# Performance work log

Hardware: AMD Instinct MI355X
Metric: run time of the kernel (lower is better)

Reference implementation:

```python
import jax, jax.numpy as jnp
import numpy as np

D_MODEL, N_HEADS, D_FF = 1024, 16, 4096
D_HEAD = D_MODEL // N_HEADS
B, S = 2, 2048
EPS = 1e-5


def setup_inputs() -> dict:
    key = jax.random.key(0)
    ks = jax.random.split(key, 12)
    sd = 1.0 / np.sqrt(D_MODEL)
    return {
        "x": jax.random.normal(ks[0], (B, S, D_MODEL), jnp.float32),
        "relative_bias": jax.random.normal(ks[1], (1, N_HEADS, S, S), jnp.float32),
        # attention projections, stored as (in, out) so y = x @ W
        "wq": jax.random.normal(ks[2], (D_MODEL, D_MODEL), jnp.float32) * sd,
        "wk": jax.random.normal(ks[3], (D_MODEL, D_MODEL), jnp.float32) * sd,
        "wv": jax.random.normal(ks[4], (D_MODEL, D_MODEL), jnp.float32) * sd,
        "wo": jax.random.normal(ks[5], (D_MODEL, D_MODEL), jnp.float32) * sd,
        "wo_b": jnp.zeros((D_MODEL,), jnp.float32),
        # FFN
        "w1": jax.random.normal(ks[6], (D_MODEL, D_FF), jnp.float32) * sd,
        "b1": jnp.zeros((D_FF,), jnp.float32),
        "w2": jax.random.normal(ks[7], (D_FF, D_MODEL), jnp.float32) * (1.0 / np.sqrt(D_FF)),
        "b2": jnp.zeros((D_MODEL,), jnp.float32),
        # LayerNorms
        "ln1_g": jnp.ones((D_MODEL,), jnp.float32),
        "ln1_b": jnp.zeros((D_MODEL,), jnp.float32),
        "ln2_g": jnp.ones((D_MODEL,), jnp.float32),
        "ln2_b": jnp.zeros((D_MODEL,), jnp.float32),
    }


def _layernorm(x, g, b):
    mu = jnp.mean(x, axis=-1, keepdims=True)
    var = jnp.mean(jnp.square(x - mu), axis=-1, keepdims=True)
    return (x - mu) * jax.lax.rsqrt(var + EPS) * g + b


def _attn(x, relative_bias, wq, wk, wv, wo, wo_b):
    b, s, d = x.shape
    # (B,S,D) -> (B,H,S,Dh)
    def split_heads(t):
        return t.reshape(b, s, N_HEADS, D_HEAD).transpose(0, 2, 1, 3)
    q = split_heads(x @ wq)
    k = split_heads(x @ wk)
    v = split_heads(x @ wv)
    scores = jnp.einsum("bhqd,bhkd->bhqk", q, k) / np.sqrt(D_HEAD) + relative_bias
    attn = jax.nn.softmax(scores, axis=-1)
    ctx = jnp.einsum("bhqk,bhkd->bhqd", attn, v)
    ctx = ctx.transpose(0, 2, 1, 3).reshape(b, s, d)
    return ctx @ wo + wo_b


def _ffn(x, w1, b1, w2, b2):
    return jax.nn.gelu(x @ w1 + b1, approximate=False) @ w2 + b2


def reference(x, relative_bias, wq, wk, wv, wo, wo_b, w1, b1, w2, b2,
              ln1_g, ln1_b, ln2_g, ln2_b):
    x = x + _attn(_layernorm(x, ln1_g, ln1_b), relative_bias, wq, wk, wv, wo, wo_b)
    x = x + _ffn(_layernorm(x, ln2_g, ln2_b), w1, b1, w2, b2)
    return x
```

## Files before the change

kernel.cpp:

```cpp
#include <hip/hip_runtime.h>
#include <hip/hip_bf16.h>
#include <stdint.h>

typedef unsigned short u16;
typedef __bf16 bf16x8 __attribute__((ext_vector_type(8)));
typedef u16   u16x8  __attribute__((ext_vector_type(8)));
typedef u16   u16x4  __attribute__((ext_vector_type(4)));
typedef u16   u16x2  __attribute__((ext_vector_type(2)));
typedef float f32x4  __attribute__((ext_vector_type(4)));

__device__ __forceinline__ u16 f2bf(float f) {
  union { float f; uint32_t u; } v; v.f = f;
  uint32_t r = v.u + 0x7fffu + ((v.u >> 16) & 1u);
  return (u16)(r >> 16);
}

typedef __attribute__((address_space(1))) void gvoid_t;
typedef __attribute__((address_space(3))) void lvoid_t;
__device__ __forceinline__ void gload_lds16(const void* g, void* l) {
  __builtin_amdgcn_global_load_lds((gvoid_t*)g, (lvoid_t*)l, 16, 0, 0);
}

template<int CTRL>
__device__ __forceinline__ float dpp_f(float x) {
  int i = __builtin_bit_cast(int, x);
  i = __builtin_amdgcn_update_dpp(i, i, CTRL, 0xF, 0xF, true);
  return __builtin_bit_cast(float, i);
}
__device__ __forceinline__ float rowmax16(float x) {
  x = fmaxf(x, dpp_f<0x128>(x));
  x = fmaxf(x, dpp_f<0x124>(x));
  x = fmaxf(x, dpp_f<0x122>(x));
  x = fmaxf(x, dpp_f<0x121>(x));
  return x;
}
__device__ __forceinline__ float rowsum16(float x) {
  x += dpp_f<0x128>(x);
  x += dpp_f<0x124>(x);
  x += dpp_f<0x122>(x);
  x += dpp_f<0x121>(x);
  return x;
}

__global__ __launch_bounds__(256)
void ln_kernel(const float* __restrict__ x, const float* __restrict__ g,
               const float* __restrict__ b, u16* __restrict__ out) {
  const int row = blockIdx.x;
  const int tid = threadIdx.x;
  const float* xr = x + (size_t)row * 1024;
  f32x4 v = *(const f32x4*)&xr[tid * 4];
  float s = v[0] + v[1] + v[2] + v[3];
  float q = v[0]*v[0] + v[1]*v[1] + v[2]*v[2] + v[3]*v[3];
  #pragma unroll
  for (int o = 32; o > 0; o >>= 1) { s += __shfl_xor(s, o); q += __shfl_xor(q, o); }
  __shared__ float ss[4], qq[4];
  if ((tid & 63) == 0) { ss[tid >> 6] = s; qq[tid >> 6] = q; }
  __syncthreads();
  s = ss[0] + ss[1] + ss[2] + ss[3];
  q = qq[0] + qq[1] + qq[2] + qq[3];
  float mu = s * (1.0f / 1024.0f);
  float var = q * (1.0f / 1024.0f) - mu * mu;
  float rstd = rsqrtf(var + 1e-5f);
  u16x4 o4;
  #pragma unroll
  for (int i = 0; i < 4; ++i)
    o4[i] = f2bf((v[i] - mu) * rstd * g[tid * 4 + i] + b[tid * 4 + i]);
  *(u16x4*)&out[(size_t)row * 1024 + tid * 4] = o4;
}

__global__ __launch_bounds__(256)
void transpose_cast(const float* __restrict__ W, u16* __restrict__ Wt, int K, int N) {
  __shared__ float t[32][33];
  const int n0 = blockIdx.x * 32, k0 = blockIdx.y * 32;
  const int tx = threadIdx.x & 31, ty = threadIdx.x >> 5;
  #pragma unroll
  for (int i = 0; i < 4; ++i)
    t[ty + 8*i][tx] = W[(size_t)(k0 + ty + 8*i) * N + n0 + tx];
  __syncthreads();
  #pragma unroll
  for (int i = 0; i < 4; ++i)
    Wt[(size_t)(n0 + ty + 8*i) * K + k0 + tx] = f2bf(t[tx][ty + 8*i]);
}

template<int EPI>
__global__ __launch_bounds__(256, 2)
void gemm_bt(const u16* __restrict__ A, const u16* __restrict__ Bt,
             void* __restrict__ out, const float* __restrict__ bias,
             const float* __restrict__ resid, int M, int N, int K) {
  __shared__ u16 As[128 * 32];
  __shared__ u16 Bs[128 * 32];
  const int tid = threadIdx.x;
  const int w = tid >> 6, l = tid & 63;
  const int bm = blockIdx.x * 128, bn = blockIdx.y * 128;
  const int wr = (w >> 1) * 64, wc = (w & 1) * 64;
  const int l15 = l & 15, lhi = l >> 4;
  f32x4 acc[4][4] = {};

  const int r4 = tid >> 2;
  const int c8 = (tid & 3) * 8;
  const u16* ga0 = A  + (size_t)(bm + r4) * K + c8;
  const u16* ga1 = ga0 + (size_t)64 * K;
  const u16* gb0 = Bt + (size_t)(bn + r4) * K + c8;
  const u16* gb1 = gb0 + (size_t)64 * K;
  u16* lA0 = &As[(w * 16) * 32];
  u16* lA1 = &As[(64 + w * 16) * 32];
  u16* lB0 = &Bs[(w * 16) * 32];
  u16* lB1 = &Bs[(64 + w * 16) * 32];

  const int arow = (wr + l15) * 32 + lhi * 8;
  const int brow = (wc + l15) * 32 + lhi * 8;

  for (int k0 = 0; k0 < K; k0 += 32) {
    gload_lds16(ga0 + k0, lA0);
    gload_lds16(ga1 + k0, lA1);
    gload_lds16(gb0 + k0, lB0);
    gload_lds16(gb1 + k0, lB1);
    __syncthreads();
    bf16x8 a[4], b[4];
    #pragma unroll
    for (int m = 0; m < 4; ++m) a[m] = *(const bf16x8*)&As[arow + m * 16 * 32];
    #pragma unroll
    for (int n = 0; n < 4; ++n) b[n] = *(const bf16x8*)&Bs[brow + n * 16 * 32];
    #pragma unroll
    for (int m = 0; m < 4; ++m)
      #pragma unroll
      for (int n = 0; n < 4; ++n)
        acc[m][n] = __builtin_amdgcn_mfma_f32_16x16x32_bf16(a[m], b[n], acc[m][n], 0, 0, 0);
    __syncthreads();
  }

  #pragma unroll
  for (int m = 0; m < 4; ++m) {
    #pragma unroll
    for (int n = 0; n < 4; ++n) {
      #pragma unroll
      for (int r = 0; r < 4; ++r) {
        const int grow = bm + wr + m * 16 + lhi * 4 + r;
        const int gcol = bn + wc + n * 16 + l15;
        float vv = acc[m][n][r];
        if constexpr (EPI >= 1) vv += bias[gcol];
        if constexpr (EPI == 1) vv = 0.5f * vv * (1.0f + erff(vv * 0.70710678118f));
        if constexpr (EPI == 2) {
          vv += resid[(size_t)grow * N + gcol];
          ((float*)out)[(size_t)grow * N + gcol] = vv;
        } else {
          ((u16*)out)[(size_t)grow * N + gcol] = f2bf(vv);
        }
      }
    }
  }
}

#define SWZ(row) ((((row) & 7) ^ (((row) >> 3) & 7)) << 3)

__global__ __launch_bounds__(256)
void attn_kernel(const u16* __restrict__ qkv, const float* __restrict__ bias,
                 u16* __restrict__ ctx) {
  const int qt = blockIdx.x;
  const int bh = blockIdx.y;
  const int b = bh >> 4, h = bh & 15;
  const int tid = threadIdx.x, w = tid >> 6, l = tid & 63;
  const int l15 = l & 15, lhi = l >> 4;
  const size_t ld = 3072;
  const float L2E = 1.44269504f;

  __shared__ u16 Kl[4096];
  __shared__ u16 Vt[4096];
  __shared__ u16 Pl[4][1024];

  const u16* qp = qkv;
  const u16* kp = qkv + 1024;
  const u16* vp = qkv + 2048;

  const int key2 = (tid >> 3) * 2, dg8 = (tid & 7) * 8;
  const u16* kbase = kp + ((size_t)b * 2048 + key2) * ld + h * 64 + dg8;
  const u16* vbase = vp + ((size_t)b * 2048 + key2) * ld + h * 64 + dg8;

  bf16x8 qf0, qf1;
  {
    const u16* qrow = qp + ((size_t)b * 2048 + qt * 64 + w * 16 + l15) * ld + h * 64 + lhi * 8;
    qf0 = *(const bf16x8*)qrow;
    qf1 = *(const bf16x8*)(qrow + 32);
  }

  const float* bg0 = bias + ((size_t)h * 2048 + qt * 64 + w * 16 + lhi * 4) * 2048 + l15;

  float m_run[4], s_run[4];
  f32x4 octx[4] = {};
  #pragma unroll
  for (int r = 0; r < 4; ++r) { m_run[r] = -1e30f; s_run[r] = 0.f; }

  u16x8 kpf[2], vpf[2];
  float bf[16];

  auto load_kv = [&](int kv) {
    kpf[0] = *(const u16x8*)(kbase + (size_t)kv * ld);
    kpf[1] = *(const u16x8*)(kbase + (size_t)(kv + 1) * ld);
    vpf[0] = *(const u16x8*)(vbase + (size_t)kv * ld);
    vpf[1] = *(const u16x8*)(vbase + (size_t)(kv + 1) * ld);
  };
  auto load_bias = [&](int kv) {
    #pragma unroll
    for (int r = 0; r < 4; ++r)
      #pragma unroll
      for (int nf = 0; nf < 4; ++nf)
        bf[r * 4 + nf] = bg0[(size_t)r * 2048 + kv + nf * 16];
  };
  auto store_kv = [&]() {
    *(u16x8*)&Kl[(key2)     * 64 + (dg8 ^ SWZ(key2))]     = kpf[0];
    *(u16x8*)&Kl[(key2 + 1) * 64 + (dg8 ^ SWZ(key2 + 1))] = kpf[1];
    #pragma unroll
    for (int i = 0; i < 8; ++i) {
      const int d = dg8 + i;
      u16x2 vq = { vpf[0][i], vpf[1][i] };
      *(u16x2*)&Vt[d * 64 + (key2 ^ SWZ(d))] = vq;
    }
  };

  load_kv(0);
  load_bias(0);
  store_kv();
  __syncthreads();

  for (int it = 0; it < 32; ++it) {
    const int kv0 = it * 64;
    const bool pf = it < 31;
    if (pf) load_kv(kv0 + 64);

    f32x4 sa[4] = {};
    #pragma unroll
    for (int nf = 0; nf < 4; ++nf) {
      const int row = nf * 16 + l15;
      const int s = SWZ(row);
      bf16x8 kf0 = *(const bf16x8*)&Kl[row * 64 + ((lhi * 8) ^ s)];
      bf16x8 kf1 = *(const bf16x8*)&Kl[row * 64 + ((32 + lhi * 8) ^ s)];
      sa[nf] = __builtin_amdgcn_mfma_f32_16x16x32_bf16(qf0, kf0, sa[nf], 0, 0, 0);
      sa[nf] = __builtin_amdgcn_mfma_f32_16x16x32_bf16(qf1, kf1, sa[nf], 0, 0, 0);
    }

    float p[4][4];
    #pragma unroll
    for (int r = 0; r < 4; ++r)
      #pragma unroll
      for (int nf = 0; nf < 4; ++nf)
        p[r][nf] = fmaf(sa[nf][r], 0.125f, bf[r * 4 + nf]);
    if (pf) load_bias(kv0 + 64);

    #pragma unroll
    for (int r = 0; r < 4; ++r) {
      float mx = fmaxf(fmaxf(p[r][0], p[r][1]), fmaxf(p[r][2], p[r][3]));
      mx = rowmax16(mx);
      if (mx > m_run[r] + 5.545177f) {
        const float fs = exp2f((m_run[r] - mx) * L2E);
        s_run[r] *= fs;
        #pragma unroll
        for (int nf = 0; nf < 4; ++nf) octx[nf][r] *= fs;
        m_run[r] = mx;
      }
      const float nml = -m_run[r] * L2E;
      float e0 = exp2f(fmaf(p[r][0], L2E, nml));
      float e1 = exp2f(fmaf(p[r][1], L2E, nml));
      float e2 = exp2f(fmaf(p[r][2], L2E, nml));
      float e3 = exp2f(fmaf(p[r][3], L2E, nml));
      p[r][0] = e0; p[r][1] = e1; p[r][2] = e2; p[r][3] = e3;
      s_run[r] += rowsum16((e0 + e1) + (e2 + e3));
    }

    #pragma unroll
    for (int r = 0; r < 4; ++r) {
      const int row = lhi * 4 + r;
      const int s = SWZ(row);
      #pragma unroll
      for (int nf = 0; nf < 4; ++nf)
        Pl[w][row * 64 + ((nf * 16 + l15) ^ s)] = f2bf(p[r][nf]);
    }

    #pragma unroll
    for (int ks = 0; ks < 2; ++ks) {
      bf16x8 pa = *(const bf16x8*)&Pl[w][l15 * 64 + ((ks * 32 + lhi * 8) ^ SWZ(l15))];
      #pragma unroll
      for (int nf = 0; nf < 4; ++nf) {
        const int row = nf * 16 + l15;
        bf16x8 bv = *(const bf16x8*)&Vt[row * 64 + ((ks * 32 + lhi * 8) ^ SWZ(row))];
        octx[nf] = __builtin_amdgcn_mfma_f32_16x16x32_bf16(pa, bv, octx[nf], 0, 0, 0);
      }
    }

    __syncthreads();
    if (pf) store_kv();
    __syncthreads();
  }

  float inv[4];
  #pragma unroll
  for (int r = 0; r < 4; ++r) inv[r] = 1.0f / s_run[r];
  #pragma unroll
  for (int nf = 0; nf < 4; ++nf)
    #pragma unroll
    for (int r = 0; r < 4; ++r) {
      const int grow = b * 2048 + qt * 64 + w * 16 + lhi * 4 + r;
      const int gcol = h * 64 + nf * 16 + l15;
      ctx[(size_t)grow * 1024 + gcol] = f2bf(octx[nf][r] * inv[r]);
    }
}

extern "C" void kernel_launch(void* const* d_in, const int* in_sizes, int n_in,
                              void* d_out, int out_size, void* d_ws, size_t ws_size,
                              hipStream_t stream) {
  const float* x    = (const float*)d_in[0];
  const float* rb   = (const float*)d_in[1];
  const float* wq   = (const float*)d_in[2];
  const float* wk   = (const float*)d_in[3];
  const float* wv   = (const float*)d_in[4];
  const float* wo   = (const float*)d_in[5];
  const float* wo_b = (const float*)d_in[6];
  const float* w1   = (const float*)d_in[7];
  const float* b1   = (const float*)d_in[8];
  const float* w2   = (const float*)d_in[9];
  const float* b2   = (const float*)d_in[10];
  const float* ln1g = (const float*)d_in[11];
  const float* ln1b = (const float*)d_in[12];
  const float* ln2g = (const float*)d_in[13];
  const float* ln2b = (const float*)d_in[14];

  char* ws = (char*)d_ws;
  u16*   xn    = (u16*)(ws + 0);
  u16*   qkvb  = (u16*)(ws + (8u << 20));
  u16*   hbuf  = (u16*)(ws + (8u << 20));
  u16*   ctxb  = (u16*)(ws + (32u << 20));
  float* x1    = (float*)(ws + (40u << 20));
  u16*   wqkvt = (u16*)(ws + (56u << 20));
  u16*   wot   = (u16*)(ws + (62u << 20));
  u16*   w1t   = (u16*)(ws + (64u << 20));
  u16*   w2t   = (u16*)(ws + (72u << 20));

  transpose_cast<<<dim3(32, 32),  256, 0, stream>>>(wq, wqkvt,               1024, 1024);
  transpose_cast<<<dim3(32, 32),  256, 0, stream>>>(wk, wqkvt + 1024 * 1024, 1024, 1024);
  transpose_cast<<<dim3(32, 32),  256, 0, stream>>>(wv, wqkvt + 2048 * 1024, 1024, 1024);
  transpose_cast<<<dim3(32, 32),  256, 0, stream>>>(wo, wot,                 1024, 1024);
  transpose_cast<<<dim3(128, 32), 256, 0, stream>>>(w1, w1t,                 1024, 4096);
  transpose_cast<<<dim3(32, 128), 256, 0, stream>>>(w2, w2t,                 4096, 1024);

  ln_kernel<<<4096, 256, 0, stream>>>(x, ln1g, ln1b, xn);
  gemm_bt<0><<<dim3(32, 24), 256, 0, stream>>>(xn, wqkvt, qkvb, nullptr, nullptr, 4096, 3072, 1024);
  attn_kernel<<<dim3(32, 32), 256, 0, stream>>>(qkvb, rb, ctxb);
  gemm_bt<2><<<dim3(32, 8), 256, 0, stream>>>(ctxb, wot, x1, wo_b, x, 4096, 1024, 1024);
  ln_kernel<<<4096, 256, 0, stream>>>(x1, ln2g, ln2b, xn);
  gemm_bt<1><<<dim3(32, 32), 256, 0, stream>>>(xn, w1t, hbuf, b1, nullptr, 4096, 4096, 1024);
  gemm_bt<2><<<dim3(32, 8), 256, 0, stream>>>(hbuf, w2t, (float*)d_out, b2, x1, 4096, 1024, 4096);

  (void)in_sizes; (void)n_in; (void)out_size; (void)ws_size;
}
```

Measured before the change: 402.2 us.

## Double-buffer K/V shared tiles in attention and drop one barrier per iteration

Doubles the LDS K and V buffers so the next tile is stored into the other buffer while the current one is consumed, and issues global loads two tiles ahead. This removes one of the two __syncthreads per loop iteration and gives more latency hiding for the K/V loads. It also switches the bias loads to pointer increments and replaces the manual bf16 rounding with a native cast. The cost is more LDS use per block, which may reduce occupancy, and longer live ranges for the prefetch registers.

New measurement: 399.5 us. No clear change (-0.7%).

```diff
diff --git a/kernel.cpp b/kernel.cpp
--- a/kernel.cpp
+++ b/kernel.cpp
@@ -164,8 +164,8 @@
   const size_t ld = 3072;
   const float L2E = 1.44269504f;
 
-  __shared__ u16 Kl[4096];
-  __shared__ u16 Vt[4096];
+  __shared__ u16 Kl[2][4096];
+  __shared__ u16 Vt[2][4096];
   __shared__ u16 Pl[4][1024];
 
   const u16* qp = qkv;
@@ -184,6 +184,10 @@
   }
 
   const float* bg0 = bias + ((size_t)h * 2048 + qt * 64 + w * 16 + lhi * 4) * 2048 + l15;
+  const float* bp0 = bg0;
+  const float* bp1 = bg0 + 2048;
+  const float* bp2 = bg0 + 4096;
+  const float* bp3 = bg0 + 6144;
 
   float m_run[4], s_run[4];
   f32x4 octx[4] = {};
@@ -199,41 +203,42 @@
     vpf[0] = *(const u16x8*)(vbase + (size_t)kv * ld);
     vpf[1] = *(const u16x8*)(vbase + (size_t)(kv + 1) * ld);
   };
-  auto load_bias = [&](int kv) {
-    #pragma unroll
-    for (int r = 0; r < 4; ++r)
-      #pragma unroll
-      for (int nf = 0; nf < 4; ++nf)
-        bf[r * 4 + nf] = bg0[(size_t)r * 2048 + kv + nf * 16];
+  auto load_bias = [&]() {
+    bf[0]  = bp0[0];  bf[1]  = bp0[16]; bf[2]  = bp0[32]; bf[3]  = bp0[48];
+    bf[4]  = bp1[0];  bf[5]  = bp1[16]; bf[6]  = bp1[32]; bf[7]  = bp1[48];
+    bf[8]  = bp2[0];  bf[9]  = bp2[16]; bf[10] = bp2[32]; bf[11] = bp2[48];
+    bf[12] = bp3[0];  bf[13] = bp3[16]; bf[14] = bp3[32]; bf[15] = bp3[48];
+    bp0 += 64; bp1 += 64; bp2 += 64; bp3 += 64;
   };
-  auto store_kv = [&]() {
-    *(u16x8*)&Kl[(key2)     * 64 + (dg8 ^ SWZ(key2))]     = kpf[0];
-    *(u16x8*)&Kl[(key2 + 1) * 64 + (dg8 ^ SWZ(key2 + 1))] = kpf[1];
+  auto store_kv = [&](u16* Kd, u16* Vd) {
+    *(u16x8*)&Kd[(key2)     * 64 + (dg8 ^ SWZ(key2))]     = kpf[0];
+    *(u16x8*)&Kd[(key2 + 1) * 64 + (dg8 ^ SWZ(key2 + 1))] = kpf[1];
     #pragma unroll
     for (int i = 0; i < 8; ++i) {
       const int d = dg8 + i;
       u16x2 vq = { vpf[0][i], vpf[1][i] };
-      *(u16x2*)&Vt[d * 64 + (key2 ^ SWZ(d))] = vq;
+      *(u16x2*)&Vd[d * 64 + (key2 ^ SWZ(d))] = vq;
     }
   };
 
   load_kv(0);
-  load_bias(0);
-  store_kv();
+  load_bias();
+  store_kv(Kl[0], Vt[0]);
+  load_kv(64);
   __syncthreads();
 
   for (int it = 0; it < 32; ++it) {
-    const int kv0 = it * 64;
-    const bool pf = it < 31;
-    if (pf) load_kv(kv0 + 64);
+    const int cur = it & 1, nxt = cur ^ 1;
+    if (it < 31) store_kv(Kl[nxt], Vt[nxt]);
+    if (it < 30) load_kv((it + 2) * 64);
 
     f32x4 sa[4] = {};
     #pragma unroll
     for (int nf = 0; nf < 4; ++nf) {
       const int row = nf * 16 + l15;
       const int s = SWZ(row);
-      bf16x8 kf0 = *(const bf16x8*)&Kl[row * 64 + ((lhi * 8) ^ s)];
-      bf16x8 kf1 = *(const bf16x8*)&Kl[row * 64 + ((32 + lhi * 8) ^ s)];
+      bf16x8 kf0 = *(const bf16x8*)&Kl[cur][row * 64 + ((lhi * 8) ^ s)];
+      bf16x8 kf1 = *(const bf16x8*)&Kl[cur][row * 64 + ((32 + lhi * 8) ^ s)];
       sa[nf] = __builtin_amdgcn_mfma_f32_16x16x32_bf16(qf0, kf0, sa[nf], 0, 0, 0);
       sa[nf] = __builtin_amdgcn_mfma_f32_16x16x32_bf16(qf1, kf1, sa[nf], 0, 0, 0);
     }
@@ -244,7 +249,7 @@
       #pragma unroll
       for (int nf = 0; nf < 4; ++nf)
         p[r][nf] = fmaf(sa[nf][r], 0.125f, bf[r * 4 + nf]);
-    if (pf) load_bias(kv0 + 64);
+    if (it < 31) load_bias();
 
     #pragma unroll
     for (int r = 0; r < 4; ++r) {
@@ -272,7 +277,8 @@
       const int s = SWZ(row);
       #pragma unroll
       for (int nf = 0; nf < 4; ++nf)
-        Pl[w][row * 64 + ((nf * 16 + l15) ^ s)] = f2bf(p[r][nf]);
+        Pl[w][row * 64 + ((nf * 16 + l15) ^ s)] =
+            __builtin_bit_cast(u16, (__bf16)p[r][nf]);
     }
 
     #pragma unroll
@@ -281,13 +287,11 @@
       #pragma unroll
       for (int nf = 0; nf < 4; ++nf) {
         const int row = nf * 16 + l15;
-        bf16x8 bv = *(const bf16x8*)&Vt[row * 64 + ((ks * 32 + lhi * 8) ^ SWZ(row))];
+        bf16x8 bv = *(const bf16x8*)&Vt[cur][row * 64 + ((ks * 32 + lhi * 8) ^ SWZ(row))];
         octx[nf] = __builtin_amdgcn_mfma_f32_16x16x32_bf16(pa, bv, octx[nf], 0, 0, 0);
       }
     }
 
-    __syncthreads();
-    if (pf) store_kv();
     __syncthreads();
   }
 
```
